# Performance work log

Hardware: AMD Instinct MI355X
Metric: run time of the kernel (lower is better)

The kernel has to match this reference:

```python
import jax, jax.numpy as jnp
import numpy as np

# DAG: node -> list of children; node 0 is the stem output, node 6 is the cell output.
GRAPH = {1: [0], 2: [0, 1], 3: [1, 2], 4: [2, 3], 5: [3, 4], 6: [4, 5]}
OUTPUT_NODE = 6


def conv3x3(x, w, b):
    # x: [N,C,H,W], w: [O,I,3,3], b: [O]; stride 1, SAME padding (PyTorch Conv2d pad=1)
    y = jax.lax.conv_general_dilated(
        x, w, window_strides=(1, 1), padding='SAME',
        dimension_numbers=('NCHW', 'OIHW', 'NCHW'))
    return y + b[None, :, None, None]


def setup_inputs() -> dict:
    key = jax.random.key(0)
    k_x, k_w0, k_b0, k_wn, k_bn = jax.random.split(key, 5)
    scale = 0.05  # keep activations bounded through 7 stacked convs
    return {
        'x': jax.random.normal(k_x, (8, 64, 64, 64), dtype=jnp.float32),
        'W0': jax.random.normal(k_w0, (128, 64, 3, 3), dtype=jnp.float32) * scale,
        'b0': jax.random.normal(k_b0, (128,), dtype=jnp.float32) * scale,
        'Wn': jax.random.normal(k_wn, (6, 128, 128, 3, 3), dtype=jnp.float32) * scale,
        'bn': jax.random.normal(k_bn, (6, 128), dtype=jnp.float32) * scale,
    }


def reference(x, W0, b0, Wn, bn):
    # activations[0] = layers['0'](x)
    acts = {0: conv3x3(x, W0, b0)}
    # DFS with memoization over a DAG == topological evaluation of nodes 1..6.
    # Each node n sums its OWN conv (weights Wn[n-1]) applied to every child activation.
    for node in range(1, OUTPUT_NODE + 1):
        w, b = Wn[node - 1], bn[node - 1]
        out = None
        for child in GRAPH[node]:
            y = conv3x3(acts[child], w, b)
            out = y if out is None else out + y
        acts[node] = out
    return acts[OUTPUT_NODE]
```

## Files before the change

kernel.cpp:

```cpp
#include <hip/hip_runtime.h>


typedef __bf16 bf16x8 __attribute__((ext_vector_type(8)));
typedef float f32x4 __attribute__((ext_vector_type(4)));

union U4 { uint4 u; bf16x8 b; };

__device__ inline unsigned pk_bf16(float lo, float hi) {
  unsigned r;
  asm volatile("v_cvt_pk_bf16_f32 %0, %1, %2" : "=v"(r) : "v"(lo), "v"(hi));
  return r;
}

__device__ inline unsigned addpk(unsigned a, unsigned b) {
  float alo = __builtin_bit_cast(float, a << 16);
  float ahi = __builtin_bit_cast(float, a & 0xFFFF0000u);
  float blo = __builtin_bit_cast(float, b << 16);
  float bhi = __builtin_bit_cast(float, b & 0xFFFF0000u);
  return pk_bf16(alo + blo, ahi + bhi);
}

__device__ inline uint4 addpk4(uint4 a, uint4 b) {
  return make_uint4(addpk(a.x, b.x), addpk(a.y, b.y), addpk(a.z, b.z), addpk(a.w, b.w));
}

__device__ __forceinline__ void gload16(const unsigned* g, unsigned* l) {
  __builtin_amdgcn_global_load_lds(
      (const __attribute__((address_space(1))) unsigned*)(g),
      (__attribute__((address_space(3))) unsigned*)(l), 16, 0, 0);
}

template <int N>
__device__ __forceinline__ void waitcnt_vm() {
  if constexpr (N == 0) asm volatile("s_waitcnt vmcnt(0)" ::: "memory");
  else if constexpr (N == 1) asm volatile("s_waitcnt vmcnt(1)" ::: "memory");
  else asm volatile("s_waitcnt vmcnt(2)" ::: "memory");
}

#define WB_WORDS 479232
__global__ void repack_w(const float* __restrict__ W0,
                         const float* __restrict__ Wn,
                         unsigned* __restrict__ Wb) {
  unsigned gid = blockIdx.x * 256 + threadIdx.x;
  if (gid >= WB_WORDS) return;
  const float* src;
  int CIN, c, r, j;
  if (gid < 36864) {
    src = W0; CIN = 64;
    c = gid >> 11; int w = gid & 2047; r = w >> 5; j = w & 31;
  } else {
    unsigned g = gid - 36864;
    int s = g / 73728; unsigned r2 = g % 73728;
    src = Wn + (size_t)s * 147456; CIN = 128;
    c = r2 >> 12; int w = r2 & 4095; r = w >> 6; j = w & 63;
  }
  int ochalf = c / 9, tap = c % 9;
  int dy = tap / 3, dx = tap % 3;
  int icpair = j ^ ((r & 7) << 2);
  int oc = ochalf * 64 + r;
  size_t base = (((size_t)oc * CIN + 2 * icpair) * 3 + dy) * 3 + dx;
  Wb[gid] = pk_bf16(src[base], src[base + 9]);
}

__global__ void zero_halos(unsigned* __restrict__ B0, unsigned* __restrict__ B1,
                           unsigned* __restrict__ B2, unsigned* __restrict__ T) {
  unsigned gid = blockIdx.x * 256 + threadIdx.x;
  if (gid >= 116480) return;
  unsigned* buf; int CW; unsigned u;
  if (gid < 99840) {
    buf = gid < 33280 ? B0 : (gid < 66560 ? B1 : B2);
    u = gid % 33280; CW = 64;
  } else {
    buf = T; u = gid - 99840; CW = 32;
  }
  int per_n = 65 * CW;
  int n = u / per_n;
  unsigned v = u % per_n;
  int pix = (v * 4) / CW, cw = (v * 4) % CW;
  int row, col;
  if (pix < 66) { row = 0; col = pix; }
  else if (pix < 132) { row = 65; col = pix - 66; }
  else if (pix < 196) { row = pix - 131; col = 0; }
  else { row = pix - 195; col = 65; }
  *(uint4*)&buf[((((size_t)n * 66 + row) * 66 + col) * CW) + cw] =
      make_uint4(0, 0, 0, 0);
}

__global__ void transform_x(const float* __restrict__ x, unsigned* __restrict__ T) {
  __shared__ float xl[64][65];
  int n = blockIdx.y, h = blockIdx.x, tid = threadIdx.x;
#pragma unroll
  for (int k = 0; k < 16; ++k) {
    int idx = tid + k * 256;
    int ic = idx >> 6, w = idx & 63;
    xl[w][ic] = x[(((size_t)n * 64 + ic) * 64 + h) * 64 + w];
  }
  __syncthreads();
#pragma unroll
  for (int k = 0; k < 8; ++k) {
    int idx = tid + k * 256;
    int w = idx >> 5, icp = idx & 31;
    unsigned v = pk_bf16(xl[w][icp * 2], xl[w][icp * 2 + 1]);
    int wp = w + 1;
    int pos = icp ^ ((wp & 7) << 2);
    T[(((size_t)n * 66 + (h + 1)) * 66 + wp) * 32 + pos] = v;
  }
}

template <int CIN, bool DUAL, bool OUTF32>
__global__ __launch_bounds__(512, 2) void conv_stage(
    const unsigned* __restrict__ in0, const unsigned* __restrict__ in1,
    const unsigned* __restrict__ wb, const float* __restrict__ bias,
    float bmult, void* __restrict__ outp) {
  constexpr int WPP = CIN / 2;
  constexpr int CHW = 64 * WPP;
  constexpr int WL = CHW / 2048;
  constexpr int ROWW = 66 * WPP;
  constexpr int ACTW = 6 * ROWW;
  constexpr int ALDS_W = (ACTW > 16384) ? ACTW : 16384;
  constexpr int ACT_U4 = ACTW / 4;
  constexpr int AJ = (ACT_U4 + 511) / 512;
  constexpr int KCW = CIN / 64;

  __shared__ unsigned Alds[ALDS_W];
  __shared__ unsigned Wlds[3][CHW];

  const int tid = threadIdx.x;
  const int lane = tid & 63;
  const int wav = tid >> 6;
  const int wr = wav >> 1;
  const int kh = wav & 1;
  const int l15 = lane & 15, q = lane >> 4;
  const int bid = blockIdx.x;
  const int n = bid & 7;
  const int ochalf = (bid >> 3) & 1;
  const int hq = bid >> 4;
  const int h0 = hq * 4;

  const unsigned* wbase = wb + (size_t)ochalf * 9 * CHW;

#pragma unroll
  for (int s = 0; s < WL; ++s)
    gload16(wbase + s * 2048 + tid * 4, &Wlds[0][s * 2048 + wav * 256]);
#pragma unroll
  for (int s = 0; s < WL; ++s)
    gload16(wbase + CHW + s * 2048 + tid * 4, &Wlds[1][s * 2048 + wav * 256]);

  {
    const size_t abase = ((size_t)n * 66 + h0) * ROWW;
    const uint4* g0 = (const uint4*)(in0 + abase);
    const uint4* g1 = (const uint4*)(in1 + abase);
#pragma unroll
    for (int j = 0; j < AJ; ++j) {
      int i = tid + j * 512;
      if (i < ACT_U4) {
        uint4 v = g0[i];
        if (DUAL) v = addpk4(v, g1[i]);
        *(uint4*)&Alds[4 * i] = v;
      }
    }
  }
  __syncthreads();

  f32x4 acc[4][4];
#pragma unroll
  for (int m = 0; m < 4; ++m)
#pragma unroll
    for (int p = 0; p < 4; ++p) acc[m][p] = (f32x4)0.f;

#pragma unroll
  for (int t = 0; t < 9; ++t) {
    if (t < 8) waitcnt_vm<WL>();
    else waitcnt_vm<0>();
    __builtin_amdgcn_s_barrier();
    __builtin_amdgcn_sched_barrier(0);

    const unsigned* WB = Wlds[t % 3];
    const int dy = t / 3, dx = t % 3;
    const int arow = (wr + dy) * 66;

    __builtin_amdgcn_s_setprio(1);
#pragma unroll
    for (int kc2 = 0; kc2 < KCW; ++kc2) {
      const int kc = kh * KCW + kc2;
      bf16x8 a[4];
#pragma unroll
      for (int m = 0; m < 4; ++m) {
        int r = m * 16 + l15;
        U4 u;
        u.u = *(const uint4*)&WB[r * WPP + ((kc * 16 + q * 4) ^ ((r & 7) << 2))];
        a[m] = u.b;
      }
      bf16x8 b[4];
#pragma unroll
      for (int p = 0; p < 4; ++p) {
        int col = p * 16 + l15 + dx;
        U4 u;
        u.u = *(const uint4*)&Alds[(arow + col) * WPP +
                                   ((kc * 16 + q * 4) ^ ((col & 7) << 2))];
        b[p] = u.b;
      }
#pragma unroll
      for (int m = 0; m < 4; ++m)
#pragma unroll
        for (int p = 0; p < 4; ++p)
          acc[m][p] =
              __builtin_amdgcn_mfma_f32_16x16x32_bf16(a[m], b[p], acc[m][p], 0, 0, 0);
    }
    __builtin_amdgcn_s_setprio(0);
    __builtin_amdgcn_sched_barrier(0);

    if (t + 2 < 9) {
#pragma unroll
      for (int s = 0; s < WL; ++s)
        gload16(wbase + (size_t)(t + 2) * CHW + s * 2048 + tid * 4,
                &Wlds[(t + 2) % 3][s * 2048 + wav * 256]);
    }
    __builtin_amdgcn_sched_barrier(0);
  }

  __syncthreads();
  float* R = (float*)Alds;
  if (kh) {
#pragma unroll
    for (int m = 0; m < 4; ++m)
#pragma unroll
      for (int p = 0; p < 4; ++p)
        *(f32x4*)&R[(wr * 16 + m * 4 + p) * 256 + lane * 4] = acc[m][p];
  }
  __syncthreads();
  if (kh) return;
#pragma unroll
  for (int m = 0; m < 4; ++m)
#pragma unroll
    for (int p = 0; p < 4; ++p) {
      f32x4 o = *(const f32x4*)&R[(wr * 16 + m * 4 + p) * 256 + lane * 4];
      acc[m][p] += o;
    }

  const int obase = ochalf * 64;
  if (OUTF32) {
    float* out = (float*)outp;
#pragma unroll
    for (int m = 0; m < 4; ++m) {
      int oc0 = obase + m * 16 + q * 4;
      float4 bb = *(const float4*)&bias[oc0];
#pragma unroll
      for (int p = 0; p < 4; ++p) {
        int w = p * 16 + l15;
#pragma unroll
        for (int j = 0; j < 4; ++j)
          out[(((size_t)n * 128 + oc0 + j) * 64 + (h0 + wr)) * 64 + w] =
              acc[m][p][j] + ((const float*)&bb)[j] * bmult;
      }
    }
  } else {
    unsigned* out = (unsigned*)outp;
#pragma unroll
    for (int m = 0; m < 4; ++m) {
      int oc0 = obase + m * 16 + q * 4;
      float4 bb = *(const float4*)&bias[oc0];
      int icp0 = oc0 >> 1;
#pragma unroll
      for (int p = 0; p < 4; ++p) {
        int w = p * 16 + l15;
        int wp = w + 1;
        unsigned lo = pk_bf16(acc[m][p][0] + bb.x * bmult, acc[m][p][1] + bb.y * bmult);
        unsigned hi = pk_bf16(acc[m][p][2] + bb.z * bmult, acc[m][p][3] + bb.w * bmult);
        int pos = icp0 ^ ((wp & 7) << 2);
        size_t base = (((size_t)n * 66 + (h0 + 1 + wr)) * 66 + wp) * 64;
        *(uint2*)&out[base + pos] = make_uint2(lo, hi);
      }
    }
  }
}

extern "C" void kernel_launch(void* const* d_in, const int* in_sizes, int n_in,
                              void* d_out, int out_size, void* d_ws,
                              size_t ws_size, hipStream_t stream) {
  const float* x = (const float*)d_in[0];
  const float* W0 = (const float*)d_in[1];
  const float* b0 = (const float*)d_in[2];
  const float* Wn = (const float*)d_in[3];
  const float* bn = (const float*)d_in[4];

  const size_t ACTB = (size_t)8 * 66 * 66 * 64;
  const size_t TW = (size_t)8 * 66 * 66 * 32;
  unsigned* B0 = (unsigned*)d_ws;
  unsigned* B1 = B0 + ACTB;
  unsigned* B2 = B1 + ACTB;
  unsigned* T = B2 + ACTB;
  unsigned* Wb = T + TW;

  zero_halos<<<455, 256, 0, stream>>>(B0, B1, B2, T);
  repack_w<<<WB_WORDS / 256, 256, 0, stream>>>(W0, Wn, Wb);
  transform_x<<<dim3(64, 8), 256, 0, stream>>>(x, T);

  dim3 grid(256), blk(512);
  const unsigned* Wnode = Wb + 36864;
  const size_t NW = 73728;

  conv_stage<64, false, false><<<grid, blk, 0, stream>>>(T, T, Wb, b0, 1.f, B0);
  conv_stage<128, false, false><<<grid, blk, 0, stream>>>(B0, B0, Wnode, bn + 0, 1.f, B1);
  conv_stage<128, true, false><<<grid, blk, 0, stream>>>(B0, B1, Wnode + 1 * NW, bn + 128, 2.f, B2);
  conv_stage<128, true, false><<<grid, blk, 0, stream>>>(B1, B2, Wnode + 2 * NW, bn + 256, 2.f, B0);
  conv_stage<128, true, false><<<grid, blk, 0, stream>>>(B2, B0, Wnode + 3 * NW, bn + 384, 2.f, B1);
  conv_stage<128, true, false><<<grid, blk, 0, stream>>>(B0, B1, Wnode + 4 * NW, bn + 512, 2.f, B2);
  conv_stage<128, true, true><<<grid, blk, 0, stream>>>(B1, B2, Wnode + 5 * NW, bn + 640, 2.f, d_out);

  (void)in_sizes; (void)n_in; (void)out_size; (void)ws_size;
}
```

Measured before the change: 115.3 us.

## Fuse setup kernels and defer last two activation rows past first tap

Merges the three setup kernels (halo zeroing, weight repack, input transform) into one launch to cut launch overhead. In the conv stage, the last two rows of the activation tile are loaded into registers early and written to LDS after the first tap's MFMAs, since tap 0 (dy=0) only reads rows 0-3. This overlaps part of the activation load with compute. It costs extra registers and needs a wait on both LDS and global counters at each tap barrier.

```diff
diff --git a/kernel.cpp b/kernel.cpp
--- a/kernel.cpp
+++ b/kernel.cpp
@@ -31,79 +31,97 @@
 }
 
 template <int N>
-__device__ __forceinline__ void waitcnt_vm() {
-  if constexpr (N == 0) asm volatile("s_waitcnt vmcnt(0)" ::: "memory");
-  else if constexpr (N == 1) asm volatile("s_waitcnt vmcnt(1)" ::: "memory");
-  else asm volatile("s_waitcnt vmcnt(2)" ::: "memory");
+__device__ __forceinline__ void waitcnt_vm_lgkm() {
+  if constexpr (N == 0)
+    asm volatile("s_waitcnt vmcnt(0) lgkmcnt(0)" ::: "memory");
+  else if constexpr (N == 1)
+    asm volatile("s_waitcnt vmcnt(1) lgkmcnt(0)" ::: "memory");
+  else
+    asm volatile("s_waitcnt vmcnt(2) lgkmcnt(0)" ::: "memory");
 }
 
 #define WB_WORDS 479232
-__global__ void repack_w(const float* __restrict__ W0,
-                         const float* __restrict__ Wn,
-                         unsigned* __restrict__ Wb) {
-  unsigned gid = blockIdx.x * 256 + threadIdx.x;
-  if (gid >= WB_WORDS) return;
-  const float* src;
-  int CIN, c, r, j;
-  if (gid < 36864) {
-    src = W0; CIN = 64;
-    c = gid >> 11; int w = gid & 2047; r = w >> 5; j = w & 31;
-  } else {
-    unsigned g = gid - 36864;
-    int s = g / 73728; unsigned r2 = g % 73728;
-    src = Wn + (size_t)s * 147456; CIN = 128;
-    c = r2 >> 12; int w = r2 & 4095; r = w >> 6; j = w & 63;
-  }
-  int ochalf = c / 9, tap = c % 9;
-  int dy = tap / 3, dx = tap % 3;
-  int icpair = j ^ ((r & 7) << 2);
-  int oc = ochalf * 64 + r;
-  size_t base = (((size_t)oc * CIN + 2 * icpair) * 3 + dy) * 3 + dx;
-  Wb[gid] = pk_bf16(src[base], src[base + 9]);
-}
-
-__global__ void zero_halos(unsigned* __restrict__ B0, unsigned* __restrict__ B1,
-                           unsigned* __restrict__ B2, unsigned* __restrict__ T) {
-  unsigned gid = blockIdx.x * 256 + threadIdx.x;
-  if (gid >= 116480) return;
-  unsigned* buf; int CW; unsigned u;
-  if (gid < 99840) {
-    buf = gid < 33280 ? B0 : (gid < 66560 ? B1 : B2);
-    u = gid % 33280; CW = 64;
-  } else {
-    buf = T; u = gid - 99840; CW = 32;
-  }
-  int per_n = 65 * CW;
-  int n = u / per_n;
-  unsigned v = u % per_n;
-  int pix = (v * 4) / CW, cw = (v * 4) % CW;
-  int row, col;
-  if (pix < 66) { row = 0; col = pix; }
-  else if (pix < 132) { row = 65; col = pix - 66; }
-  else if (pix < 196) { row = pix - 131; col = 0; }
-  else { row = pix - 195; col = 65; }
-  *(uint4*)&buf[((((size_t)n * 66 + row) * 66 + col) * CW) + cw] =
-      make_uint4(0, 0, 0, 0);
-}
-
-__global__ void transform_x(const float* __restrict__ x, unsigned* __restrict__ T) {
-  __shared__ float xl[64][65];
-  int n = blockIdx.y, h = blockIdx.x, tid = threadIdx.x;
-#pragma unroll
-  for (int k = 0; k < 16; ++k) {
-    int idx = tid + k * 256;
-    int ic = idx >> 6, w = idx & 63;
-    xl[w][ic] = x[(((size_t)n * 64 + ic) * 64 + h) * 64 + w];
-  }
-  __syncthreads();
-#pragma unroll
-  for (int k = 0; k < 8; ++k) {
-    int idx = tid + k * 256;
-    int w = idx >> 5, icp = idx & 31;
-    unsigned v = pk_bf16(xl[w][icp * 2], xl[w][icp * 2 + 1]);
-    int wp = w + 1;
-    int pos = icp ^ ((wp & 7) << 2);
-    T[(((size_t)n * 66 + (h + 1)) * 66 + wp) * 32 + pos] = v;
+
+__global__ __launch_bounds__(512) void setup_all(
+    const float* __restrict__ x, const float* __restrict__ W0,
+    const float* __restrict__ Wn, unsigned* __restrict__ B0,
+    unsigned* __restrict__ B1, unsigned* __restrict__ B2,
+    unsigned* __restrict__ T, unsigned* __restrict__ Wb) {
+  __shared__ float xl[2 * 64 * 65];
+  const int tid = threadIdx.x;
+  const int bid = blockIdx.x;
+  const int n = bid & 7;
+
+#pragma unroll
+  for (int it = 0; it < 4; ++it) {
+    unsigned gid = (unsigned)bid * 512 + tid + it * 131072u;
+    if (gid < WB_WORDS) {
+      const float* src;
+      int CIN, c, r, j;
+      if (gid < 36864) {
+        src = W0; CIN = 64;
+        c = gid >> 11; int w = gid & 2047; r = w >> 5; j = w & 31;
+      } else {
+        unsigned g2 = gid - 36864;
+        int s = g2 / 73728; unsigned r2 = g2 % 73728;
+        src = Wn + (size_t)s * 147456; CIN = 128;
+        c = r2 >> 12; int w = r2 & 4095; r = w >> 6; j = w & 63;
+      }
+      int ochalf = c / 9, tap = c % 9;
+      int dy = tap / 3, dx = tap % 3;
+      int icpair = j ^ ((r & 7) << 2);
+      int oc = ochalf * 64 + r;
+      size_t base = (((size_t)oc * CIN + 2 * icpair) * 3 + dy) * 3 + dx;
+      Wb[gid] = pk_bf16(src[base], src[base + 9]);
+    }
+  }
+
+  {
+    unsigned gid = (unsigned)bid * 512 + tid;
+    if (gid < 116480) {
+      unsigned* buf; int CW; unsigned u;
+      if (gid < 99840) {
+        buf = gid < 33280 ? B0 : (gid < 66560 ? B1 : B2);
+        u = gid % 33280; CW = 64;
+      } else {
+        buf = T; u = gid - 99840; CW = 32;
+      }
+      int per_n = 65 * CW;
+      int nn = u / per_n;
+      unsigned v = u % per_n;
+      int pix = (v * 4) / CW, cw = (v * 4) % CW;
+      int row, col;
+      if (pix < 66) { row = 0; col = pix; }
+      else if (pix < 132) { row = 65; col = pix - 66; }
+      else if (pix < 196) { row = pix - 131; col = 0; }
+      else { row = pix - 195; col = 65; }
+      *(uint4*)&buf[((((size_t)nn * 66 + row) * 66 + col) * CW) + cw] =
+          make_uint4(0, 0, 0, 0);
+    }
+  }
+
+  {
+    int hh = bid >> 3;
+    int sub = tid >> 8;
+    int t8 = tid & 255;
+    int h = hh * 2 + sub;
+#pragma unroll
+    for (int k = 0; k < 16; ++k) {
+      int idx = t8 + k * 256;
+      int ic = idx >> 6, w = idx & 63;
+      xl[(sub * 64 + w) * 65 + ic] = x[(((size_t)n * 64 + ic) * 64 + h) * 64 + w];
+    }
+    __syncthreads();
+#pragma unroll
+    for (int k = 0; k < 8; ++k) {
+      int idx = t8 + k * 256;
+      int w = idx >> 5, icp = idx & 31;
+      unsigned v = pk_bf16(xl[(sub * 64 + w) * 65 + icp * 2],
+                           xl[(sub * 64 + w) * 65 + icp * 2 + 1]);
+      int wp = w + 1;
+      int pos = icp ^ ((wp & 7) << 2);
+      T[(((size_t)n * 66 + (h + 1)) * 66 + wp) * 32 + pos] = v;
+    }
   }
 }
 
@@ -118,8 +136,10 @@
   constexpr int ROWW = 66 * WPP;
   constexpr int ACTW = 6 * ROWW;
   constexpr int ALDS_W = (ACTW > 16384) ? ACTW : 16384;
-  constexpr int ACT_U4 = ACTW / 4;
-  constexpr int AJ = (ACT_U4 + 511) / 512;
+  constexpr int R4_U4 = 4 * ROWW / 4;
+  constexpr int R2_U4 = 2 * ROWW / 4;
+  constexpr int AJ4 = (R4_U4 + 511) / 512;
+  constexpr int LJ = (R2_U4 + 511) / 512;
   constexpr int KCW = CIN / 64;
 
   __shared__ unsigned Alds[ALDS_W];
@@ -138,6 +158,19 @@
   const int h0 = hq * 4;
 
   const unsigned* wbase = wb + (size_t)ochalf * 9 * CHW;
+  const size_t abase = ((size_t)n * 66 + h0) * ROWW;
+  const uint4* g0 = (const uint4*)(in0 + abase);
+  const uint4* g1 = (const uint4*)(in1 + abase);
+
+  uint4 l0[LJ], l1[LJ];
+#pragma unroll
+  for (int j = 0; j < LJ; ++j) {
+    int i = tid + j * 512;
+    if (i < R2_U4) {
+      l0[j] = g0[R4_U4 + i];
+      if (DUAL) l1[j] = g1[R4_U4 + i];
+    }
+  }
 
 #pragma unroll
   for (int s = 0; s < WL; ++s)
@@ -146,18 +179,13 @@
   for (int s = 0; s < WL; ++s)
     gload16(wbase + CHW + s * 2048 + tid * 4, &Wlds[1][s * 2048 + wav * 256]);
 
-  {
-    const size_t abase = ((size_t)n * 66 + h0) * ROWW;
-    const uint4* g0 = (const uint4*)(in0 + abase);
-    const uint4* g1 = (const uint4*)(in1 + abase);
-#pragma unroll
-    for (int j = 0; j < AJ; ++j) {
-      int i = tid + j * 512;
-      if (i < ACT_U4) {
-        uint4 v = g0[i];
-        if (DUAL) v = addpk4(v, g1[i]);
-        *(uint4*)&Alds[4 * i] = v;
-      }
+#pragma unroll
+  for (int j = 0; j < AJ4; ++j) {
+    int i = tid + j * 512;
+    if (i < R4_U4) {
+      uint4 v = g0[i];
+      if (DUAL) v = addpk4(v, g1[i]);
+      *(uint4*)&Alds[4 * i] = v;
     }
   }
   __syncthreads();
@@ -170,8 +198,8 @@
 
 #pragma unroll
   for (int t = 0; t < 9; ++t) {
-    if (t < 8) waitcnt_vm<WL>();
-    else waitcnt_vm<0>();
+    if (t < 8) waitcnt_vm_lgkm<WL>();
+    else waitcnt_vm_lgkm<0>();
     __builtin_amdgcn_s_barrier();
     __builtin_amdgcn_sched_barrier(0);
 
@@ -209,6 +237,18 @@
     }
     __builtin_amdgcn_s_setprio(0);
     __builtin_amdgcn_sched_barrier(0);
+
+    if (t == 0) {
+#pragma unroll
+      for (int j = 0; j < LJ; ++j) {
+        int i = tid + j * 512;
+        if (i < R2_U4) {
+          uint4 v = l0[j];
+          if (DUAL) v = addpk4(v, l1[j]);
+          *(uint4*)&Alds[4 * (R4_U4 + i)] = v;
+        }
+      }
+    }
 
     if (t + 2 < 9) {
 #pragma unroll
@@ -292,9 +332,7 @@
   unsigned* T = B2 + ACTB;
   unsigned* Wb = T + TW;
 
-  zero_halos<<<455, 256, 0, stream>>>(B0, B1, B2, T);
-  repack_w<<<WB_WORDS / 256, 256, 0, stream>>>(W0, Wn, Wb);
-  transform_x<<<dim3(64, 8), 256, 0, stream>>>(x, T);
+  setup_all<<<256, 512, 0, stream>>>(x, W0, Wn, B0, B1, B2, T, Wb);
 
   dim3 grid(256), blk(512);
   const unsigned* Wnode = Wb + 36864;
```

Measured after the change: 108.4 us. 1.06x faster.
